# Kernel tuning notes

Hardware: AMD Instinct MI355X
Metric: run time of the kernel (lower is better)

Reference implementation:

```python
import jax, jax.numpy as jnp
import numpy as np

B, L, D = 2048, 200, 128
N_ITEMS = 100000


def _lin(k, fan_in, fan_out):
    s = 1.0 / np.sqrt(fan_in)
    kw, kb = jax.random.split(k)
    w = jax.random.uniform(kw, (fan_in, fan_out), jnp.float32, -s, s)
    b = jax.random.uniform(kb, (fan_out,), jnp.float32, -s, s)
    return w, b


def setup_inputs() -> dict:
    key = jax.random.key(0)
    ks = jax.random.split(key, 12)
    item_emb = jax.random.normal(ks[0], (N_ITEMS, D), jnp.float32).at[0].set(0.0)  # padding_idx=0
    item_bias_tab = jax.random.normal(ks[1], (N_ITEMS, 1), jnp.float32).at[0].set(0.0)
    aw1, ab1 = _lin(ks[2], 3 * D, 128)
    aw2, ab2 = _lin(ks[3], 128, 64)
    afw, afb = _lin(ks[4], 64, 1)
    nw, nb = _lin(ks[5], D, D)
    dw1, db1 = _lin(ks[6], 3 * D, 512)
    dw2, db2 = _lin(ks[7], 512, 256)
    dw3, db3 = _lin(ks[8], 256, 128)
    fw, fb = _lin(ks[9], 128, 1)
    in_item_id = jax.random.randint(ks[10], (B, L), 0, N_ITEMS, dtype=jnp.int32)
    item_id = jax.random.randint(ks[11], (B,), 0, N_ITEMS, dtype=jnp.int32)
    return dict(in_item_id=in_item_id, item_id=item_id, item_emb=item_emb,
                item_bias_tab=item_bias_tab, aw1=aw1, ab1=ab1, aw2=aw2, ab2=ab2,
                afw=afw, afb=afb, nw=nw, nb=nb, dw1=dw1, db1=db1, dw2=dw2, db2=db2,
                dw3=dw3, db3=db3, fw=fw, fb=fb)


def reference(in_item_id, item_id, item_emb, item_bias_tab,
              aw1, ab1, aw2, ab2, afw, afb, nw, nb,
              dw1, db1, dw2, db2, dw3, db3, fw, fb):
    sig = jax.nn.sigmoid
    seq_emb = item_emb[in_item_id]          # [B, L, D]
    target_emb = item_emb[item_id]          # [B, D]
    item_bias = item_bias_tab[item_id][:, 0]  # [B]

    t = target_emb[:, None, :]              # [B, 1, D] broadcast over L
    key = jnp.concatenate((jnp.broadcast_to(t, seq_emb.shape),
                           t * seq_emb,
                           t - seq_emb), axis=-1)  # [B, L, 3D]

    # feed-forward (DIN) attention scorer: MLP(key) -> scalar score per position
    h = sig(key @ aw1 + ab1)
    h = sig(h @ aw2 + ab2)
    score = (h @ afw + afb)[..., 0]         # [B, L]
    score = jnp.where(in_item_id == 0, 0.0, score)  # key_padding_mask, softmax=False
    attn_seq = jnp.einsum('bl,bld->bd', score, seq_emb)  # [B, D]

    attn_seq = attn_seq @ nw + nb           # norm Linear
    cat_emb = jnp.concatenate((attn_seq, target_emb, target_emb * attn_seq), axis=-1)  # [B, 3D]
    g = sig(cat_emb @ dw1 + db1)
    g = sig(g @ dw2 + db2)
    g = sig(g @ dw3 + db3)
    out = (g @ fw + fb)[:, 0]               # [B]
    return out + item_bias
```

## Files before the change

### kernel.cpp

```cpp
#include <hip/hip_runtime.h>
#include <hip/hip_bf16.h>
#include <stdint.h>

typedef __attribute__((ext_vector_type(8))) short bf8;
typedef __attribute__((ext_vector_type(4))) short bf4;
typedef __attribute__((ext_vector_type(4))) float f32x4;

#define MFMA16(a,b,c) __builtin_amdgcn_mfma_f32_16x16x32_bf16(a,b,c,0,0,0)

__device__ __forceinline__ unsigned short f2bf(float x){
  unsigned int u = __builtin_bit_cast(unsigned int, x);
  u = u + 0x7FFFu + ((u >> 16) & 1u);
  return (unsigned short)(u >> 16);
}
__device__ __forceinline__ unsigned short f2bfb(float x){
  __hip_bfloat16 h = __float2bfloat16(x);
  return __builtin_bit_cast(unsigned short, h);
}
__device__ __forceinline__ float bf2f(unsigned short h){
  unsigned int u = ((unsigned int)h) << 16;
  return __builtin_bit_cast(float, u);
}
__device__ __forceinline__ float sigm(float x){
  return 1.0f / (1.0f + __expf(-x));
}
__device__ __forceinline__ int swzu(int row, int k, int Kd8){
  return (row*Kd8 + ((k>>3) ^ (row & 7)))*8 + (k & 7);
}

__global__ void k_prep(const float* __restrict__ aw1, const float* __restrict__ aw2,
                       const float* __restrict__ nw, const float* __restrict__ dw1,
                       const float* __restrict__ dw2, const float* __restrict__ dw3,
                       unsigned short* __restrict__ WbT, unsigned short* __restrict__ WcT,
                       unsigned short* __restrict__ Wsum, unsigned short* __restrict__ A2T,
                       unsigned short* __restrict__ NWT, unsigned short* __restrict__ D1T,
                       unsigned short* __restrict__ D2T, unsigned short* __restrict__ D3T)
{
  int n = blockIdx.x*256 + threadIdx.x;
  int stride = gridDim.x*256;
  for (int i = n; i < 16384; i += stride){
    int j = i >> 7, k = i & 127;
    WbT[i] = f2bf(aw1[(128+k)*128 + j]);
    WcT[i] = f2bf(aw1[(256+k)*128 + j]);
  }
  for (int i = n; i < 16384; i += stride){
    int j = i >> 7, k = i & 127;
    Wsum[i] = f2bf(aw1[k*128 + j] + aw1[(256+k)*128 + j]);
  }
  for (int i = n; i < 8192; i += stride){
    int j = i >> 7, k = i & 127;
    A2T[i] = f2bf(aw2[k*64 + j]);
  }
  for (int i = n; i < 16384; i += stride){
    int j = i >> 7, k = i & 127;
    NWT[i] = f2bf(nw[k*128 + j]);
  }
  for (int i = n; i < 196608; i += stride){
    int j = i / 384, k = i - j*384;
    D1T[i] = f2bf(dw1[k*512 + j]);
  }
  for (int i = n; i < 131072; i += stride){
    int j = i >> 9, k = i & 511;
    D2T[i] = f2bf(dw2[k*256 + j]);
  }
  for (int i = n; i < 32768; i += stride){
    int j = i >> 8, k = i & 255;
    D3T[i] = f2bf(dw3[k*128 + j]);
  }
}

__global__ __launch_bounds__(256, 4) void k_attn(
    const int* __restrict__ in_ids, const int* __restrict__ item_id,
    const float* __restrict__ emb,
    const float* __restrict__ ab1, const float* __restrict__ ab2v,
    const float* __restrict__ afw, const float* __restrict__ afb,
    const unsigned short* __restrict__ WbT, const unsigned short* __restrict__ WcT,
    const unsigned short* __restrict__ Wsum, const unsigned short* __restrict__ A2T,
    float* __restrict__ attn_raw)
{
  __shared__ __align__(16) unsigned short sS[32*128];
  __shared__ __align__(16) unsigned short sH[32*128];
  __shared__ float sT[128];
  __shared__ float sC0[128];
  __shared__ float sP2[2][128];
  __shared__ float sPart[4][32];
  __shared__ int   sIds[32];

  const int b = blockIdx.x;
  const int tid = threadIdx.x;
  const int wave = tid >> 6, lane = tid & 63;
  const int lr = lane & 15, lg = lane >> 4;

  const int tgt = item_id[b];
  if (tid < 128) sT[tid] = emb[(size_t)tgt*128 + tid];
  __syncthreads();

  {
    int j = tid & 127, hf = tid >> 7;
    const unsigned short* wsrow = Wsum + j*128 + hf*64;
    float p = 0.f;
    #pragma unroll
    for (int c = 0; c < 8; ++c){
      bf8 wv = *(const bf8*)(wsrow + c*8);
      #pragma unroll
      for (int e = 0; e < 8; ++e)
        p += sT[hf*64 + c*8 + e] * bf2f((unsigned short)wv[e]);
    }
    sP2[hf][j] = p;
  }
  __syncthreads();
  if (tid < 128) sC0[tid] = ab1[tid] + sP2[0][tid] + sP2[1][tid];

  bf8 wfrag[2][4];
  {
    const float4* sT4 = (const float4*)sT;
    #pragma unroll
    for (int mt = 0; mt < 2; ++mt){
      int j = (wave + mt*4)*16 + lr;
      #pragma unroll
      for (int kk = 0; kk < 4; ++kk){
        bf8 wb = *(const bf8*)(WbT + j*128 + kk*32 + lg*8);
        bf8 wc = *(const bf8*)(WcT + j*128 + kk*32 + lg*8);
        float4 t0 = sT4[kk*8 + lg*2];
        float4 t1 = sT4[kk*8 + lg*2 + 1];
        float tv[8] = {t0.x,t0.y,t0.z,t0.w,t1.x,t1.y,t1.z,t1.w};
        bf8 o;
        #pragma unroll
        for (int e = 0; e < 8; ++e)
          o[e] = (short)f2bfb(tv[e]*bf2f((unsigned short)wb[e]) - bf2f((unsigned short)wc[e]));
        wfrag[mt][kk] = o;
      }
    }
  }
  bf8 a2frag[4];
  #pragma unroll
  for (int kk = 0; kk < 4; ++kk)
    a2frag[kk] = *(const bf8*)(A2T + (wave*16+lr)*128 + kk*32 + lg*8);

  float b2r[4], afr[4];
  #pragma unroll
  for (int i = 0; i < 4; ++i){
    int j2 = wave*16 + lg*4 + i;
    b2r[i] = ab2v[j2];
    afr[i] = afw[j2];
  }
  const float afbv = afb[0];
  __syncthreads();
  float c0r[2][4];
  #pragma unroll
  for (int mt = 0; mt < 2; ++mt)
    #pragma unroll
    for (int i = 0; i < 4; ++i)
      c0r[mt][i] = sC0[(wave + mt*4)*16 + lg*4 + i];

  float facc8[8] = {0,0,0,0,0,0,0,0};
  const bf8* S8 = (const bf8*)sS;
  const bf8* H8 = (const bf8*)sH;
  const int rg = tid >> 4, cg = tid & 15;
  const int sxm = lr & 7;

  for (int rt = 0; rt < 7; ++rt){
    __syncthreads();
    #pragma unroll
    for (int qq = 0; qq < 2; ++qq){
      int c2 = qq*256 + tid;
      int r = c2 >> 4, ch = c2 & 15;
      int l = rt*32 + r;
      int id = (l < 200) ? in_ids[b*200 + l] : 0;
      if (ch == 0) sIds[r] = id;
      const float* src = emb + (size_t)id*128 + ch*8;
      float4 v0 = *(const float4*)src;
      float4 v1 = *(const float4*)(src + 4);
      bf8 o;
      o[0]=(short)f2bfb(v0.x); o[1]=(short)f2bfb(v0.y); o[2]=(short)f2bfb(v0.z); o[3]=(short)f2bfb(v0.w);
      o[4]=(short)f2bfb(v1.x); o[5]=(short)f2bfb(v1.y); o[6]=(short)f2bfb(v1.z); o[7]=(short)f2bfb(v1.w);
      ((bf8*)sS)[r*16 + (ch ^ (r & 7))] = o;
    }
    __syncthreads();
    f32x4 acc1[2][2] = {};
    #pragma unroll
    for (int kk = 0; kk < 4; ++kk){
      int kx = (kk*4 + lg) ^ sxm;
      bf8 s0 = S8[lr*16 + kx];
      bf8 s1 = S8[(16+lr)*16 + kx];
      acc1[0][0] = MFMA16(wfrag[0][kk], s0, acc1[0][0]);
      acc1[0][1] = MFMA16(wfrag[0][kk], s1, acc1[0][1]);
      acc1[1][0] = MFMA16(wfrag[1][kk], s0, acc1[1][0]);
      acc1[1][1] = MFMA16(wfrag[1][kk], s1, acc1[1][1]);
    }
    #pragma unroll
    for (int mt = 0; mt < 2; ++mt)
      #pragma unroll
      for (int nt = 0; nt < 2; ++nt){
        int r = nt*16 + lr;
        int j0 = (wave + mt*4)*16 + lg*4;
        bf4 q4;
        #pragma unroll
        for (int i = 0; i < 4; ++i)
          q4[i] = (short)f2bfb(sigm(acc1[mt][nt][i] + c0r[mt][i]));
        int idx = (r*16 + ((j0 >> 3) ^ (r & 7)))*8 + (j0 & 7);
        *(bf4*)(sH + idx) = q4;
      }
    __syncthreads();
    f32x4 acc2[2] = {};
    #pragma unroll
    for (int kk = 0; kk < 4; ++kk){
      int kx = (kk*4 + lg) ^ sxm;
      bf8 h0 = H8[lr*16 + kx];
      bf8 h1f = H8[(16+lr)*16 + kx];
      acc2[0] = MFMA16(a2frag[kk], h0, acc2[0]);
      acc2[1] = MFMA16(a2frag[kk], h1f, acc2[1]);
    }
    float part0 = 0.f, part1 = 0.f;
    #pragma unroll
    for (int i = 0; i < 4; ++i){
      part0 += sigm(acc2[0][i] + b2r[i]) * afr[i];
      part1 += sigm(acc2[1][i] + b2r[i]) * afr[i];
    }
    part0 += __shfl_xor(part0, 16); part0 += __shfl_xor(part0, 32);
    part1 += __shfl_xor(part1, 16); part1 += __shfl_xor(part1, 32);
    if (lg == 0){ sPart[wave][lr] = part0; sPart[wave][16+lr] = part1; }
    __syncthreads();
    #pragma unroll
    for (int q = 0; q < 2; ++q){
      int r = rg*2 + q;
      int l = rt*32 + r;
      float sc = sPart[0][r] + sPart[1][r] + sPart[2][r] + sPart[3][r] + afbv;
      sc = (l < 200 && sIds[r] != 0) ? sc : 0.f;
      bf8 v = S8[r*16 + (cg ^ (r & 7))];
      #pragma unroll
      for (int e = 0; e < 8; ++e)
        facc8[e] += sc * bf2f((unsigned short)v[e]);
    }
  }
  __syncthreads();
  float* red = (float*)sS;
  #pragma unroll
  for (int e = 0; e < 8; ++e) red[tid*8 + e] = facc8[e];
  __syncthreads();
  if (tid < 128){
    float s = 0.f;
    #pragma unroll
    for (int g = 0; g < 16; ++g) s += red[g*128 + tid];
    attn_raw[(size_t)b*128 + tid] = s;
  }
}

__global__ __launch_bounds__(256) void k_deep(
    const int* __restrict__ item_id, const float* __restrict__ emb,
    const float* __restrict__ bias_tab,
    const float* __restrict__ nbv,
    const float* __restrict__ db1, const float* __restrict__ db2,
    const float* __restrict__ db3, const float* __restrict__ fw,
    const float* __restrict__ fb,
    const unsigned short* __restrict__ NWT, const unsigned short* __restrict__ D1T,
    const unsigned short* __restrict__ D2T, const unsigned short* __restrict__ D3T,
    const float* __restrict__ attn_raw, float* __restrict__ out)
{
  __shared__ __align__(16) unsigned short sA[16*128];
  __shared__ float sTf[16*128];
  __shared__ __align__(16) unsigned short sCat[16*384];
  __shared__ __align__(16) unsigned short sG1[16*512];
  __shared__ __align__(16) unsigned short sG2[16*256];
  __shared__ __align__(16) unsigned short sG3[16*128];
  __shared__ float sNB[128], sDB1[512], sDB2[256], sDB3[128], sFWd[128];
  __shared__ float sBias[16];

  const int r0 = blockIdx.x * 16;
  const int tid = threadIdx.x;
  const int wave = tid >> 6, lane = tid & 63;
  const int lr = lane & 15, lg = lane >> 4;
  const int sx = lr & 7;

  if (tid < 128){ sNB[tid] = nbv[tid]; sDB3[tid] = db3[tid]; sFWd[tid] = fw[tid]; }
  for (int i = tid; i < 512; i += 256) sDB1[i] = db1[i];
  sDB2[tid] = db2[tid];
  if (tid < 16) sBias[tid] = bias_tab[item_id[r0 + tid]];

  {
    int r = tid >> 4, ch = tid & 15;
    const float* asrc = attn_raw + (size_t)(r0 + r)*128 + ch*8;
    float4 v0 = *(const float4*)asrc;
    float4 v1 = *(const float4*)(asrc + 4);
    bf8 o;
    o[0]=(short)f2bf(v0.x); o[1]=(short)f2bf(v0.y); o[2]=(short)f2bf(v0.z); o[3]=(short)f2bf(v0.w);
    o[4]=(short)f2bf(v1.x); o[5]=(short)f2bf(v1.y); o[6]=(short)f2bf(v1.z); o[7]=(short)f2bf(v1.w);
    ((bf8*)sA)[r*16 + (ch ^ (r & 7))] = o;
    int id = item_id[r0 + r];
    const float* tsrc = emb + (size_t)id*128 + ch*8;
    float4 t0 = *(const float4*)tsrc;
    float4 t1 = *(const float4*)(tsrc + 4);
    *(float4*)(sTf + r*128 + ch*8)     = t0;
    *(float4*)(sTf + r*128 + ch*8 + 4) = t1;
  }
  __syncthreads();

  {
    const bf8* A8 = (const bf8*)sA;
    #pragma unroll
    for (int c = 0; c < 2; ++c){
      int ct = wave + c*4;
      f32x4 acc = {};
      #pragma unroll
      for (int kk = 0; kk < 4; ++kk){
        int kx = (kk*4 + lg) ^ sx;
        bf8 af = A8[lr*16 + kx];
        bf8 bw = *(const bf8*)(NWT + (ct*16+lr)*128 + kk*32 + lg*8);
        acc = MFMA16(af, bw, acc);
      }
      int col = ct*16 + lr;
      float nbc = sNB[col];
      #pragma unroll
      for (int i = 0; i < 4; ++i){
        int r = lg*4 + i;
        float x = acc[i] + nbc;
        float tv = sTf[r*128 + col];
        sCat[swzu(r, col,      48)] = f2bf(x);
        sCat[swzu(r, 128+col,  48)] = f2bf(tv);
        sCat[swzu(r, 256+col,  48)] = f2bf(tv * x);
      }
    }
  }
  __syncthreads();
  {
    const bf8* C8 = (const bf8*)sCat;
    #pragma unroll
    for (int c = 0; c < 8; ++c){
      int ct = wave + c*4;
      f32x4 acc = {};
      #pragma unroll
      for (int kk = 0; kk < 12; ++kk){
        int kx = (kk*4 + lg) ^ sx;
        bf8 af = C8[lr*48 + kx];
        bf8 bw = *(const bf8*)(D1T + (size_t)(ct*16+lr)*384 + kk*32 + lg*8);
        acc = MFMA16(af, bw, acc);
      }
      int col = ct*16 + lr;
      float bb = sDB1[col];
      #pragma unroll
      for (int i = 0; i < 4; ++i)
        sG1[swzu(lg*4 + i, col, 64)] = f2bf(sigm(acc[i] + bb));
    }
  }
  __syncthreads();
  {
    const bf8* G8 = (const bf8*)sG1;
    #pragma unroll
    for (int c = 0; c < 4; ++c){
      int ct = wave + c*4;
      f32x4 acc = {};
      #pragma unroll
      for (int kk = 0; kk < 16; ++kk){
        int kx = (kk*4 + lg) ^ sx;
        bf8 af = G8[lr*64 + kx];
        bf8 bw = *(const bf8*)(D2T + (size_t)(ct*16+lr)*512 + kk*32 + lg*8);
        acc = MFMA16(af, bw, acc);
      }
      int col = ct*16 + lr;
      float bb = sDB2[col];
      #pragma unroll
      for (int i = 0; i < 4; ++i)
        sG2[swzu(lg*4 + i, col, 32)] = f2bf(sigm(acc[i] + bb));
    }
  }
  __syncthreads();
  {
    const bf8* G8 = (const bf8*)sG2;
    #pragma unroll
    for (int c = 0; c < 2; ++c){
      int ct = wave + c*4;
      f32x4 acc = {};
      #pragma unroll
      for (int kk = 0; kk < 8; ++kk){
        int kx = (kk*4 + lg) ^ sx;
        bf8 af = G8[lr*32 + kx];
        bf8 bw = *(const bf8*)(D3T + (size_t)(ct*16+lr)*256 + kk*32 + lg*8);
        acc = MFMA16(af, bw, acc);
      }
      int col = ct*16 + lr;
      float bb = sDB3[col];
      #pragma unroll
      for (int i = 0; i < 4; ++i)
        sG3[swzu(lg*4 + i, col, 16)] = f2bf(sigm(acc[i] + bb));
    }
  }
  __syncthreads();
  if (tid < 128){
    int r = tid >> 3, seg = tid & 7;
    float p = 0.f;
    #pragma unroll
    for (int c = 0; c < 16; ++c)
      p += bf2f(sG3[swzu(r, seg*16 + c, 16)]) * sFWd[seg*16 + c];
    p += __shfl_xor(p, 1);
    p += __shfl_xor(p, 2);
    p += __shfl_xor(p, 4);
    if (seg == 0) out[r0 + r] = p + fb[0] + sBias[r];
  }
}

extern "C" void kernel_launch(void* const* d_in, const int* in_sizes, int n_in,
                              void* d_out, int out_size, void* d_ws, size_t ws_size,
                              hipStream_t stream) {
  const int*   in_ids   = (const int*)d_in[0];
  const int*   item_id  = (const int*)d_in[1];
  const float* emb      = (const float*)d_in[2];
  const float* bias_tab = (const float*)d_in[3];
  const float* aw1 = (const float*)d_in[4];
  const float* ab1 = (const float*)d_in[5];
  const float* aw2 = (const float*)d_in[6];
  const float* ab2 = (const float*)d_in[7];
  const float* afw = (const float*)d_in[8];
  const float* afb = (const float*)d_in[9];
  const float* nw  = (const float*)d_in[10];
  const float* nb  = (const float*)d_in[11];
  const float* dw1 = (const float*)d_in[12];
  const float* db1 = (const float*)d_in[13];
  const float* dw2 = (const float*)d_in[14];
  const float* db2 = (const float*)d_in[15];
  const float* dw3 = (const float*)d_in[16];
  const float* db3 = (const float*)d_in[17];
  const float* fw  = (const float*)d_in[18];
  const float* fb  = (const float*)d_in[19];
  float* outp = (float*)d_out;

  char* ws = (char*)d_ws;
  float* attn_raw = (float*)ws;
  unsigned short* WbT  = (unsigned short*)(ws + 1048576);
  unsigned short* WcT  = WbT  + 16384;
  unsigned short* Wsum = WcT  + 16384;
  unsigned short* A2T  = Wsum + 16384;
  unsigned short* NWT  = A2T  + 8192;
  unsigned short* D1T  = NWT  + 16384;
  unsigned short* D2T  = D1T  + 196608;
  unsigned short* D3T  = D2T  + 131072;

  hipLaunchKernelGGL(k_prep, dim3(256), dim3(256), 0, stream,
                     aw1, aw2, nw, dw1, dw2, dw3,
                     WbT, WcT, Wsum, A2T, NWT, D1T, D2T, D3T);
  hipLaunchKernelGGL(k_attn, dim3(2048), dim3(256), 0, stream,
                     in_ids, item_id, emb, ab1, ab2, afw, afb,
                     WbT, WcT, Wsum, A2T, attn_raw);
  hipLaunchKernelGGL(k_deep, dim3(128), dim3(256), 0, stream,
                     item_id, emb, bias_tab, nb, db1, db2, db3, fw, fb,
                     NWT, D1T, D2T, D3T, attn_raw, outp);
}
```

Measured before the change: 123.2 us.

## Pre-convert embedding table to bf16, prefetch gathers, widen deep MLP block

A prep kernel now converts the whole 100k x 128 fp32 embedding table to bf16 every call. The attention kernel then gathers half as many bytes per row and register-prefetches the next 32-row tile while the current one is processed. The deep MLP kernel moves from 256 to 512 threads per block so each wave handles fewer output tiles, and the sigmoid uses a hardware reciprocal. The trade-off is that the table conversion reads about 51 MB and writes about 25 MB on each call, which may cost more than the gather traffic it saves (roughly 400k rows gathered).

```diff
diff --git a/kernel.cpp b/kernel.cpp
--- a/kernel.cpp
+++ b/kernel.cpp
@@ -22,7 +22,7 @@
   return __builtin_bit_cast(float, u);
 }
 __device__ __forceinline__ float sigm(float x){
-  return 1.0f / (1.0f + __expf(-x));
+  return __builtin_amdgcn_rcpf(1.0f + __expf(-x));
 }
 __device__ __forceinline__ int swzu(int row, int k, int Kd8){
   return (row*Kd8 + ((k>>3) ^ (row & 7)))*8 + (k & 7);
@@ -31,13 +31,23 @@
 __global__ void k_prep(const float* __restrict__ aw1, const float* __restrict__ aw2,
                        const float* __restrict__ nw, const float* __restrict__ dw1,
                        const float* __restrict__ dw2, const float* __restrict__ dw3,
+                       const float* __restrict__ emb,
                        unsigned short* __restrict__ WbT, unsigned short* __restrict__ WcT,
                        unsigned short* __restrict__ Wsum, unsigned short* __restrict__ A2T,
                        unsigned short* __restrict__ NWT, unsigned short* __restrict__ D1T,
-                       unsigned short* __restrict__ D2T, unsigned short* __restrict__ D3T)
+                       unsigned short* __restrict__ D2T, unsigned short* __restrict__ D3T,
+                       unsigned short* __restrict__ EMBB)
 {
   int n = blockIdx.x*256 + threadIdx.x;
   int stride = gridDim.x*256;
+  for (int i = n; i < 1600000; i += stride){
+    const float4* s = (const float4*)(emb + (size_t)i*8);
+    float4 a = s[0], b = s[1];
+    bf8 o;
+    o[0]=(short)f2bf(a.x); o[1]=(short)f2bf(a.y); o[2]=(short)f2bf(a.z); o[3]=(short)f2bf(a.w);
+    o[4]=(short)f2bf(b.x); o[5]=(short)f2bf(b.y); o[6]=(short)f2bf(b.z); o[7]=(short)f2bf(b.w);
+    ((bf8*)EMBB)[i] = o;
+  }
   for (int i = n; i < 16384; i += stride){
     int j = i >> 7, k = i & 127;
     WbT[i] = f2bf(aw1[(128+k)*128 + j]);
@@ -71,7 +81,7 @@
 
 __global__ __launch_bounds__(256, 4) void k_attn(
     const int* __restrict__ in_ids, const int* __restrict__ item_id,
-    const float* __restrict__ emb,
+    const float* __restrict__ emb, const unsigned short* __restrict__ embb,
     const float* __restrict__ ab1, const float* __restrict__ ab2v,
     const float* __restrict__ afw, const float* __restrict__ afb,
     const unsigned short* __restrict__ WbT, const unsigned short* __restrict__ WcT,
@@ -158,23 +168,32 @@
   const bf8* H8 = (const bf8*)sH;
   const int rg = tid >> 4, cg = tid & 15;
   const int sxm = lr & 7;
+  const int chv = tid & 15;
+  const int rowq = tid >> 4;
+
+  bf8 stg0, stg1; int id0, id1;
+  {
+    id0 = in_ids[b*200 + rowq];
+    stg0 = *(const bf8*)(embb + (size_t)id0*128 + chv*8);
+    id1 = in_ids[b*200 + 16 + rowq];
+    stg1 = *(const bf8*)(embb + (size_t)id1*128 + chv*8);
+  }
 
   for (int rt = 0; rt < 7; ++rt){
     __syncthreads();
-    #pragma unroll
-    for (int qq = 0; qq < 2; ++qq){
-      int c2 = qq*256 + tid;
-      int r = c2 >> 4, ch = c2 & 15;
-      int l = rt*32 + r;
-      int id = (l < 200) ? in_ids[b*200 + l] : 0;
-      if (ch == 0) sIds[r] = id;
-      const float* src = emb + (size_t)id*128 + ch*8;
-      float4 v0 = *(const float4*)src;
-      float4 v1 = *(const float4*)(src + 4);
-      bf8 o;
-      o[0]=(short)f2bfb(v0.x); o[1]=(short)f2bfb(v0.y); o[2]=(short)f2bfb(v0.z); o[3]=(short)f2bfb(v0.w);
-      o[4]=(short)f2bfb(v1.x); o[5]=(short)f2bfb(v1.y); o[6]=(short)f2bfb(v1.z); o[7]=(short)f2bfb(v1.w);
-      ((bf8*)sS)[r*16 + (ch ^ (r & 7))] = o;
+    if (chv == 0){ sIds[rowq] = id0; sIds[16 + rowq] = id1; }
+    ((bf8*)sS)[rowq*16 + (chv ^ (rowq & 7))] = stg0;
+    {
+      int r2 = 16 + rowq;
+      ((bf8*)sS)[r2*16 + (chv ^ (r2 & 7))] = stg1;
+    }
+    if (rt < 6){
+      int l0 = (rt+1)*32 + rowq;
+      id0 = (l0 < 200) ? in_ids[b*200 + l0] : 0;
+      stg0 = *(const bf8*)(embb + (size_t)id0*128 + chv*8);
+      int l1 = l0 + 16;
+      id1 = (l1 < 200) ? in_ids[b*200 + l1] : 0;
+      stg1 = *(const bf8*)(embb + (size_t)id1*128 + chv*8);
     }
     __syncthreads();
     f32x4 acc1[2][2] = {};
@@ -246,7 +265,7 @@
   }
 }
 
-__global__ __launch_bounds__(256) void k_deep(
+__global__ __launch_bounds__(512) void k_deep(
     const int* __restrict__ item_id, const float* __restrict__ emb,
     const float* __restrict__ bias_tab,
     const float* __restrict__ nbv,
@@ -273,11 +292,11 @@
   const int sx = lr & 7;
 
   if (tid < 128){ sNB[tid] = nbv[tid]; sDB3[tid] = db3[tid]; sFWd[tid] = fw[tid]; }
-  for (int i = tid; i < 512; i += 256) sDB1[i] = db1[i];
-  sDB2[tid] = db2[tid];
+  sDB1[tid] = db1[tid];
+  if (tid < 256) sDB2[tid] = db2[tid];
   if (tid < 16) sBias[tid] = bias_tab[item_id[r0 + tid]];
 
-  {
+  if (tid < 256){
     int r = tid >> 4, ch = tid & 15;
     const float* asrc = attn_raw + (size_t)(r0 + r)*128 + ch*8;
     float4 v0 = *(const float4*)asrc;
@@ -297,36 +316,33 @@
 
   {
     const bf8* A8 = (const bf8*)sA;
-    #pragma unroll
-    for (int c = 0; c < 2; ++c){
-      int ct = wave + c*4;
-      f32x4 acc = {};
-      #pragma unroll
-      for (int kk = 0; kk < 4; ++kk){
-        int kx = (kk*4 + lg) ^ sx;
-        bf8 af = A8[lr*16 + kx];
-        bf8 bw = *(const bf8*)(NWT + (ct*16+lr)*128 + kk*32 + lg*8);
-        acc = MFMA16(af, bw, acc);
-      }
-      int col = ct*16 + lr;
-      float nbc = sNB[col];
-      #pragma unroll
-      for (int i = 0; i < 4; ++i){
-        int r = lg*4 + i;
-        float x = acc[i] + nbc;
-        float tv = sTf[r*128 + col];
-        sCat[swzu(r, col,      48)] = f2bf(x);
-        sCat[swzu(r, 128+col,  48)] = f2bf(tv);
-        sCat[swzu(r, 256+col,  48)] = f2bf(tv * x);
-      }
+    int ct = wave;
+    f32x4 acc = {};
+    #pragma unroll
+    for (int kk = 0; kk < 4; ++kk){
+      int kx = (kk*4 + lg) ^ sx;
+      bf8 af = A8[lr*16 + kx];
+      bf8 bw = *(const bf8*)(NWT + (ct*16+lr)*128 + kk*32 + lg*8);
+      acc = MFMA16(af, bw, acc);
+    }
+    int col = ct*16 + lr;
+    float nbc = sNB[col];
+    #pragma unroll
+    for (int i = 0; i < 4; ++i){
+      int r = lg*4 + i;
+      float x = acc[i] + nbc;
+      float tv = sTf[r*128 + col];
+      sCat[swzu(r, col,      48)] = f2bf(x);
+      sCat[swzu(r, 128+col,  48)] = f2bf(tv);
+      sCat[swzu(r, 256+col,  48)] = f2bf(tv * x);
     }
   }
   __syncthreads();
   {
     const bf8* C8 = (const bf8*)sCat;
     #pragma unroll
-    for (int c = 0; c < 8; ++c){
-      int ct = wave + c*4;
+    for (int c = 0; c < 4; ++c){
+      int ct = wave + c*8;
       f32x4 acc = {};
       #pragma unroll
       for (int kk = 0; kk < 12; ++kk){
@@ -346,8 +362,8 @@
   {
     const bf8* G8 = (const bf8*)sG1;
     #pragma unroll
-    for (int c = 0; c < 4; ++c){
-      int ct = wave + c*4;
+    for (int c = 0; c < 2; ++c){
+      int ct = wave + c*8;
       f32x4 acc = {};
       #pragma unroll
       for (int kk = 0; kk < 16; ++kk){
@@ -366,23 +382,20 @@
   __syncthreads();
   {
     const bf8* G8 = (const bf8*)sG2;
-    #pragma unroll
-    for (int c = 0; c < 2; ++c){
-      int ct = wave + c*4;
-      f32x4 acc = {};
-      #pragma unroll
-      for (int kk = 0; kk < 8; ++kk){
-        int kx = (kk*4 + lg) ^ sx;
-        bf8 af = G8[lr*32 + kx];
-        bf8 bw = *(const bf8*)(D3T + (size_t)(ct*16+lr)*256 + kk*32 + lg*8);
-        acc = MFMA16(af, bw, acc);
-      }
-      int col = ct*16 + lr;
-      float bb = sDB3[col];
-      #pragma unroll
-      for (int i = 0; i < 4; ++i)
-        sG3[swzu(lg*4 + i, col, 16)] = f2bf(sigm(acc[i] + bb));
-    }
+    int ct = wave;
+    f32x4 acc = {};
+    #pragma unroll
+    for (int kk = 0; kk < 8; ++kk){
+      int kx = (kk*4 + lg) ^ sx;
+      bf8 af = G8[lr*32 + kx];
+      bf8 bw = *(const bf8*)(D3T + (size_t)(ct*16+lr)*256 + kk*32 + lg*8);
+      acc = MFMA16(af, bw, acc);
+    }
+    int col = ct*16 + lr;
+    float bb = sDB3[col];
+    #pragma unroll
+    for (int i = 0; i < 4; ++i)
+      sG3[swzu(lg*4 + i, col, 16)] = f2bf(sigm(acc[i] + bb));
   }
   __syncthreads();
   if (tid < 128){
@@ -433,14 +446,15 @@
   unsigned short* D1T  = NWT  + 16384;
   unsigned short* D2T  = D1T  + 196608;
   unsigned short* D3T  = D2T  + 131072;
-
-  hipLaunchKernelGGL(k_prep, dim3(256), dim3(256), 0, stream,
-                     aw1, aw2, nw, dw1, dw2, dw3,
-                     WbT, WcT, Wsum, A2T, NWT, D1T, D2T, D3T);
+  unsigned short* EMBB = D3T  + 32768;
+
+  hipLaunchKernelGGL(k_prep, dim3(2048), dim3(256), 0, stream,
+                     aw1, aw2, nw, dw1, dw2, dw3, emb,
+                     WbT, WcT, Wsum, A2T, NWT, D1T, D2T, D3T, EMBB);
   hipLaunchKernelGGL(k_attn, dim3(2048), dim3(256), 0, stream,
-                     in_ids, item_id, emb, ab1, ab2, afw, afb,
+                     in_ids, item_id, emb, EMBB, ab1, ab2, afw, afb,
                      WbT, WcT, Wsum, A2T, attn_raw);
-  hipLaunchKernelGGL(k_deep, dim3(128), dim3(256), 0, stream,
+  hipLaunchKernelGGL(k_deep, dim3(128), dim3(512), 0, stream,
                      item_id, emb, bias_tab, nb, db1, db2, db3, fw, fb,
                      NWT, D1T, D2T, D3T, attn_raw, outp);
 }
```

New measurement: 118.3 us. 3.9% less time.
